# Optimization experiments

Hardware: AMD Instinct MI355X
Metric: run time of the kernel (lower is better)

Reference implementation:

```python
import jax, jax.numpy as jnp
import numpy as np

B, T, NX, H = 2, 2048, 1024, 16
D = NX // H  # head dim = 64
NEG = -1e9


def setup_inputs() -> dict:
    key = jax.random.key(0)
    ks = jax.random.split(key, 4)
    std = 0.02
    x = jax.random.normal(ks[0], (B, T, NX), dtype=jnp.float32)
    # non-trivial adjacency (lower-triangular) so the masking branch is active
    adj = jnp.tril(jnp.ones((T, T), dtype=jnp.float32))
    w_attn = jax.random.normal(ks[1], (NX, 3 * NX), dtype=jnp.float32) * std
    b_attn = jnp.zeros((3 * NX,), dtype=jnp.float32)
    w_proj = jax.random.normal(ks[2], (NX, NX), dtype=jnp.float32) * std
    b_proj = jnp.zeros((NX,), dtype=jnp.float32)
    w_proj1 = jax.random.normal(ks[3], (NX, NX), dtype=jnp.float32) * std
    b_proj1 = jnp.zeros((NX,), dtype=jnp.float32)
    return {"x": x, "adj": adj, "w_attn": w_attn, "b_attn": b_attn,
            "w_proj": w_proj, "b_proj": b_proj,
            "w_proj1": w_proj1, "b_proj1": b_proj1}


def reference(x, adj, w_attn, b_attn, w_proj, b_proj, w_proj1, b_proj1):
    # c_attn: fused qkv projection  [B,T,3*NX]
    qkv = jnp.einsum('btn,nm->btm', x, w_attn) + b_attn
    q, k, v = jnp.split(qkv, 3, axis=-1)  # each [B,T,NX]

    def heads(t):  # [B,T,NX] -> [B,H,T,D]
        return t.reshape(B, T, H, D).transpose(0, 2, 1, 3)

    qh, kh, vh = heads(q), heads(k), heads(v)
    # scale=False in module default: raw dot-product scores
    w = jnp.einsum('bhqd,bhkd->bhqk', qh, kh)  # [B,H,T,T]
    w = w * adj + NEG * (1.0 - adj)            # custom adjacency mask
    w = jax.nn.softmax(w, axis=-1)
    a = jnp.einsum('bhqk,bhkd->bhqd', w, vh)   # [B,H,T,D]
    a = a.transpose(0, 2, 1, 3).reshape(B, T, NX)  # merge heads
    a = jnp.einsum('btn,nm->btm', a, w_proj) + b_proj
    # residue branch: split+merge of query is identity -> c_proj_1(q)
    re = jnp.einsum('btn,nm->btm', q, w_proj1) + b_proj1
    return a + re
```

## Files before the change

### kernel.cpp

```cpp
#include <hip/hip_runtime.h>
#include <stdint.h>

typedef short s16x8 __attribute__((ext_vector_type(8)));
typedef float f32x4 __attribute__((ext_vector_type(4)));
typedef unsigned int u32x4 __attribute__((ext_vector_type(4)));

#define AS1 __attribute__((address_space(1)))
#define AS3 __attribute__((address_space(3)))

static constexpr int Bc = 2, Tc = 2048, NXc = 1024, Hc = 16;
static constexpr float NEGC = -1e9f;
static constexpr float L2E = 1.44269504088896340736f;
static constexpr float LN2 = 0.69314718055994530942f;

static __device__ __forceinline__ unsigned short f2bf(float f) {
  uint32_t u = __builtin_bit_cast(uint32_t, f);
  u += 0x7fffu + ((u >> 16) & 1u);
  return (unsigned short)(u >> 16);
}

static __device__ __forceinline__ float exp2fast(float x) {
  return __builtin_amdgcn_exp2f(x);
}

static __device__ __forceinline__ uint32_t cvt_pk_bf16(float lo, float hi) {
  uint32_t r;
  asm("v_cvt_pk_bf16_f32 %0, %1, %2" : "=v"(r) : "v"(lo), "v"(hi));
  return r;
}

static __device__ __forceinline__ void gload_lds16(const void* g, void* l) {
  __builtin_amdgcn_global_load_lds((const AS1 uint32_t*)g, (AS3 uint32_t*)l, 16, 0, 0);
}

__global__ __launch_bounds__(256) void k_prep(
    const float* __restrict__ x, unsigned short* __restrict__ xb,
    const float* __restrict__ w_attn, unsigned short* __restrict__ wattnT,
    const float* __restrict__ w_proj, const float* __restrict__ w_proj1,
    unsigned short* __restrict__ wcatT,
    const float* __restrict__ adj, unsigned char* __restrict__ tm) {
  __shared__ float tile[32][33];
  __shared__ int s_any, s_all;
  const int bid = blockIdx.x;
  const int t = threadIdx.x;

  if (bid < 4096) {
    int i = bid * 256 + t;
    float4 v = ((const float4*)x)[i];
    uint32_t lo = (uint32_t)f2bf(v.x) | ((uint32_t)f2bf(v.y) << 16);
    uint32_t hi = (uint32_t)f2bf(v.z) | ((uint32_t)f2bf(v.w) << 16);
    ((uint2*)xb)[i] = make_uint2(lo, hi);
    return;
  }
  if (bid < 9216) {
    const float* src; unsigned short* dst;
    int scols, dld, dkoff, n0, k0; float scale;
    if (bid < 7168) {
      int b = bid - 4096; n0 = (b % 96) * 32; k0 = (b / 96) * 32;
      src = w_attn; scols = 3072; dst = wattnT; dld = 1024; dkoff = 0; scale = 1.0f;
    } else if (bid < 8192) {
      int b = bid - 7168; n0 = (b & 31) * 32; k0 = (b >> 5) * 32;
      src = w_proj; scols = 1024; dst = wcatT; dld = 2048; dkoff = 0; scale = 1.0f;
    } else {
      int b = bid - 8192; n0 = (b & 31) * 32; k0 = (b >> 5) * 32;
      src = w_proj1; scols = 1024; dst = wcatT; dld = 2048; dkoff = 1024; scale = LN2;
    }
    int tx = t & 31, ty = t >> 5;
#pragma unroll
    for (int r = 0; r < 4; r++)
      tile[ty + r * 8][tx] = src[(size_t)(k0 + ty + r * 8) * scols + n0 + tx];
    __syncthreads();
#pragma unroll
    for (int r = 0; r < 4; r++) {
      int n = n0 + ty + r * 8;
      dst[(size_t)n * dld + dkoff + k0 + tx] = f2bf(tile[tx][ty + r * 8] * scale);
    }
    return;
  }
  {
    int b = bid - 9216;
    int kt = b & 31, qt = b >> 5;
    bool anyv = false, all1 = true;
#pragma unroll
    for (int i = 0; i < 4; i++) {
      int e = t * 4 + i;
      int row = e >> 4, c4 = e & 15;
      float4 v = *(const float4*)&adj[(size_t)(qt * 64 + row) * Tc + kt * 64 + c4 * 4];
      anyv |= (v.x != 0.f) | (v.y != 0.f) | (v.z != 0.f) | (v.w != 0.f);
      all1 &= (v.x == 1.f) & (v.y == 1.f) & (v.z == 1.f) & (v.w == 1.f);
    }
    if (t == 0) { s_any = 0; s_all = 1; }
    __syncthreads();
    if (anyv) s_any = 1;
    if (!all1) s_all = 0;
    __syncthreads();
    if (t == 0) tm[qt * 32 + kt] = (unsigned char)(s_any ? (s_all ? 2 : 1) : 0);
  }
}

__global__ __launch_bounds__(256) void k_gemm0(
    const unsigned short* __restrict__ A, int lda,
    const unsigned short* __restrict__ BT, int K,
    const float* __restrict__ bias0, unsigned short* __restrict__ Cb) {
  __shared__ __align__(16) unsigned short As[2][128 * 32];
  __shared__ __align__(16) unsigned short Bs[2][128 * 32];
  const int nbx = gridDim.x, nby = gridDim.y;
  const int nwg = nbx * nby;
  int id = blockIdx.y * nbx + blockIdx.x;
  id = (id & 7) * (nwg >> 3) + (id >> 3);
  const int bx = id % nbx;
  const int by = id / nbx;
  const int m0 = by * 128;
  const int n0 = bx * 128;

  const int lane = threadIdx.x & 63;
  const int w = threadIdx.x >> 6;
  const int wr = (w >> 1) * 64;
  const int wc = (w & 1) * 64;
  const int g = lane >> 4, lr = lane & 15;
  const int srow = lane >> 2;
  const int scol = lane & 3;
  f32x4 acc[4][4] = {};

  auto stage = [&](int k0, int buf) {
#pragma unroll
    for (int i = 0; i < 2; i++) {
      int c = w * 2 + i;
      int row = c * 16 + srow;
      int cs = scol ^ (row & 3);
      gload_lds16(A + (size_t)(m0 + row) * lda + k0 + cs * 8, (void*)(&As[buf][0] + c * 512));
      gload_lds16(BT + (size_t)(n0 + row) * K + k0 + cs * 8, (void*)(&Bs[buf][0] + c * 512));
    }
  };

  stage(0, 0);
  __syncthreads();

  for (int k0 = 0; k0 < K; k0 += 32) {
    const int cur = (k0 >> 5) & 1;
    if (k0 + 32 < K) stage(k0 + 32, cur ^ 1);
    s16x8 af[4], bfr[4];
#pragma unroll
    for (int m = 0; m < 4; m++) {
      int row = wr + m * 16 + lr;
      af[m] = *(const s16x8*)((const char*)&As[cur][0] + row * 64 + ((g ^ (row & 3)) * 16));
    }
#pragma unroll
    for (int n = 0; n < 4; n++) {
      int row = wc + n * 16 + lr;
      bfr[n] = *(const s16x8*)((const char*)&Bs[cur][0] + row * 64 + ((g ^ (row & 3)) * 16));
    }
#pragma unroll
    for (int m = 0; m < 4; m++)
#pragma unroll
      for (int n = 0; n < 4; n++)
        acc[m][n] = __builtin_amdgcn_mfma_f32_16x16x32_bf16(af[m], bfr[n], acc[m][n], 0, 0, 0);
    __syncthreads();
  }

#pragma unroll
  for (int m = 0; m < 4; m++) {
    int row = m0 + wr + m * 16 + g * 4;
#pragma unroll
    for (int n = 0; n < 4; n++) {
      int col = n0 + wc + n * 16 + lr;
      float bs = bias0[col];
      float sc = (col < NXc) ? L2E : 1.0f;
#pragma unroll
      for (int jj = 0; jj < 4; jj++)
        Cb[(size_t)(row + jj) * 3072 + col] = f2bf((acc[m][n][jj] + bs) * sc);
    }
  }
}

__global__ __launch_bounds__(256) void k_gemm1(
    const unsigned short* __restrict__ A, int lda,
    const unsigned short* __restrict__ A2, int lda2,
    const unsigned short* __restrict__ BT,
    const float* __restrict__ bias0, const float* __restrict__ bias1,
    float* __restrict__ Cf) {
  constexpr int K = 2048, ksplit = 1024;
  __shared__ __align__(16) unsigned short As[2][64 * 32];
  __shared__ __align__(16) unsigned short Bs[2][128 * 32];
  const int nbx = gridDim.x, nby = gridDim.y;
  const int nwg = nbx * nby;
  int id = blockIdx.y * nbx + blockIdx.x;
  id = (id & 7) * (nwg >> 3) + (id >> 3);
  const int bx = id % nbx;
  const int by = id / nbx;
  const int m0 = by * 64;
  const int n0 = bx * 128;

  const int tid = threadIdx.x;
  const int lane = tid & 63;
  const int w = tid >> 6;
  const int wr = (w >> 1) * 32;
  const int wc = (w & 1) * 64;
  const int g = lane >> 4, lr = lane & 15;
  const int srow = lane >> 2;
  const int scol = lane & 3;
  const int arow = tid >> 2;
  f32x4 acc[2][4] = {};

  auto stage = [&](int k0, int buf) {
    {
      int acs = (tid & 3) ^ (arow & 3);
      const unsigned short* ap = (k0 < ksplit)
          ? A + (size_t)(m0 + arow) * lda + k0
          : A2 + (size_t)(m0 + arow) * lda2 + (k0 - ksplit);
      gload_lds16(ap + acs * 8, (void*)(&As[buf][0] + w * 512));
    }
#pragma unroll
    for (int i = 0; i < 2; i++) {
      int c = w * 2 + i;
      int row = c * 16 + srow;
      int cs = scol ^ (row & 3);
      gload_lds16(BT + (size_t)(n0 + row) * K + k0 + cs * 8, (void*)(&Bs[buf][0] + c * 512));
    }
  };

  stage(0, 0);
  __syncthreads();

  for (int k0 = 0; k0 < K; k0 += 32) {
    const int cur = (k0 >> 5) & 1;
    if (k0 + 32 < K) stage(k0 + 32, cur ^ 1);
    s16x8 af[2], bfr[4];
#pragma unroll
    for (int m = 0; m < 2; m++) {
      int row = wr + m * 16 + lr;
      af[m] = *(const s16x8*)((const char*)&As[cur][0] + row * 64 + ((g ^ (row & 3)) * 16));
    }
#pragma unroll
    for (int n = 0; n < 4; n++) {
      int row = wc + n * 16 + lr;
      bfr[n] = *(const s16x8*)((const char*)&Bs[cur][0] + row * 64 + ((g ^ (row & 3)) * 16));
    }
#pragma unroll
    for (int m = 0; m < 2; m++)
#pragma unroll
      for (int n = 0; n < 4; n++)
        acc[m][n] = __builtin_amdgcn_mfma_f32_16x16x32_bf16(af[m], bfr[n], acc[m][n], 0, 0, 0);
    __syncthreads();
  }

#pragma unroll
  for (int m = 0; m < 2; m++) {
    int row = m0 + wr + m * 16 + g * 4;
#pragma unroll
    for (int n = 0; n < 4; n++) {
      int col = n0 + wc + n * 16 + lr;
      float bs = bias0[col] + bias1[col];
#pragma unroll
      for (int jj = 0; jj < 4; jj++)
        Cf[(size_t)(row + jj) * NXc + col] = acc[m][n][jj] + bs;
    }
  }
}

__global__ __launch_bounds__(256) void k_attn(
    const unsigned short* __restrict__ qkv,
    const float* __restrict__ adj,
    const unsigned char* __restrict__ tm,
    unsigned short* __restrict__ acat) {
  __shared__ __align__(16) unsigned short Kb[2][64 * 64];
  __shared__ __align__(16) unsigned short Vt[2][64 * 72];
  __shared__ int s_kts[34];
  __shared__ unsigned char s_tmv[32];
  __shared__ int s_nkt;

  const int bid = blockIdx.x;
  const int qt = 31 - (bid >> 5);
  const int bh = bid & 31;
  const int h = bh & 15;
  const int b = bh >> 4;
  const int q0 = qt * 64;
  const int tid = threadIdx.x;
  const int lane = tid & 63;
  const int w = tid >> 6;
  const int g = lane >> 4, lr = lane & 15;
  const int sc = tid & 7;
  const int sr = tid >> 3;
  const int kvp = 2 * sr;
  const int prp = (kvp & 32) | (((kvp >> 4) & 1) << 2) | ((kvp & 12) << 1) | (kvp & 3);

  if (w == 0) {
    int kt = lane & 31;
    unsigned char v = tm[qt * 32 + kt];
    bool act = (lane < 32) && (v != 0);
    unsigned long long mk = __ballot(act);
    int n = __popcll(mk);
    if (act) {
      int idx = __popcll(mk & ((1ull << lane) - 1));
      s_kts[idx] = kt;
      s_tmv[idx] = v;
      if (idx == n - 1) { s_kts[n] = kt; s_kts[n + 1] = kt; }
    }
    if (lane == 0) s_nkt = n;
  }

  s16x8 qf0, qf1;
  {
    size_t base = (size_t)(b * Tc + q0 + w * 16 + lr) * 3072 + h * 64 + g * 8;
    qf0 = *(const s16x8*)(qkv + base);
    qf1 = *(const s16x8*)(qkv + base + 32);
  }
  f32x4 o[4] = {};
  float lrow = 0.f;

  __syncthreads();
  const int nkt = s_nkt;
  if (nkt == 0) return;

  const unsigned short* kbase = qkv + (size_t)(b * Tc) * 3072 + 1024 + h * 64;
  const unsigned short* vbase = kbase + 1024;

  const size_t koff0 = (size_t)sr * 3072 + (sc ^ (sr & 7)) * 8;
  const size_t koff1 = (size_t)(sr + 32) * 3072 + (sc ^ (sr & 7)) * 8;
  const int kd0 = w * 1024 + lane * 16;
  const int kd1 = kd0 + 4096;
  const size_t voff0 = (size_t)kvp * 3072 + sc * 8;
  const size_t voff1 = (size_t)(kvp + 1) * 3072 + sc * 8;
  const int pcol = ((prp + sc * 8) & 63) * 2;

  s16x8 kA0, kA1, vA0, vA1;
  auto load_tile = [&](int kt) {
    const unsigned short* kb = kbase + (size_t)kt * 64 * 3072;
    const unsigned short* vb = vbase + (size_t)kt * 64 * 3072;
    kA0 = *(const s16x8*)(kb + koff0);
    kA1 = *(const s16x8*)(kb + koff1);
    vA0 = *(const s16x8*)(vb + voff0);
    vA1 = *(const s16x8*)(vb + voff1);
  };
  auto write_tile = [&](int buf) {
    *(s16x8*)((char*)&Kb[buf][0] + kd0) = kA0;
    *(s16x8*)((char*)&Kb[buf][0] + kd1) = kA1;
    char* vt = (char*)&Vt[buf][0];
#pragma unroll
    for (int j = 0; j < 8; j++) {
      int d = sc * 8 + j;
      uint32_t pk = (uint32_t)(unsigned short)vA0[j] |
                    ((uint32_t)(unsigned short)vA1[j] << 16);
      *(uint32_t*)(vt + d * 144 + pcol) = pk;
    }
  };

  load_tile(s_kts[0]);
  write_tile(0);
  load_tile(s_kts[1]);
  __syncthreads();

  for (int i = 0; i < nkt; i++) {
    const int cur = i & 1;
    const int kt = s_kts[i];
    const int tmv = s_tmv[i];
    const int kv0 = kt * 64;

    write_tile(cur ^ 1);
    load_tile(s_kts[i + 2]);

    f32x4 s[4];
    __builtin_amdgcn_s_setprio(1);
#pragma unroll
    for (int n = 0; n < 4; n++) {
      int kvr = n * 16 + lr;
      const char* kr = (const char*)&Kb[cur][0] + kvr * 128;
      s16x8 a0 = *(const s16x8*)(kr + ((g ^ (kvr & 7)) * 16));
      s16x8 a1 = *(const s16x8*)(kr + (((4 + g) ^ (kvr & 7)) * 16));
      f32x4 z = {};
      z = __builtin_amdgcn_mfma_f32_16x16x32_bf16(a0, qf0, z, 0, 0, 0);
      s[n] = __builtin_amdgcn_mfma_f32_16x16x32_bf16(a1, qf1, z, 0, 0, 0);
    }
    __builtin_amdgcn_s_setprio(0);

    if (tmv != 2) {
      const float* arow = adj + (size_t)(q0 + w * 16 + lr) * Tc + kv0;
#pragma unroll
      for (int n = 0; n < 4; n++) {
        float4 a = *(const float4*)(arow + n * 16 + 4 * g);
        s[n][0] = a.x * s[n][0] + NEGC * (1.0f - a.x);
        s[n][1] = a.y * s[n][1] + NEGC * (1.0f - a.y);
        s[n][2] = a.z * s[n][2] + NEGC * (1.0f - a.z);
        s[n][3] = a.w * s[n][3] + NEGC * (1.0f - a.w);
      }
    }

    float ps0 = 0.f, ps1 = 0.f;
#pragma unroll
    for (int n = 0; n < 4; n++) {
      float p0 = exp2fast(s[n][0]), p1 = exp2fast(s[n][1]);
      float p2 = exp2fast(s[n][2]), p3 = exp2fast(s[n][3]);
      s[n][0] = p0; s[n][1] = p1; s[n][2] = p2; s[n][3] = p3;
      ps0 += (p0 + p1); ps1 += (p2 + p3);
    }
    lrow += ps0 + ps1;

    u32x4 pw0, pw1;
    pw0.x = cvt_pk_bf16(s[0][0], s[0][1]);
    pw0.y = cvt_pk_bf16(s[0][2], s[0][3]);
    pw0.z = cvt_pk_bf16(s[1][0], s[1][1]);
    pw0.w = cvt_pk_bf16(s[1][2], s[1][3]);
    pw1.x = cvt_pk_bf16(s[2][0], s[2][1]);
    pw1.y = cvt_pk_bf16(s[2][2], s[2][3]);
    pw1.z = cvt_pk_bf16(s[3][0], s[3][1]);
    pw1.w = cvt_pk_bf16(s[3][2], s[3][3]);
    s16x8 pa0 = __builtin_bit_cast(s16x8, pw0);
    s16x8 pa1 = __builtin_bit_cast(s16x8, pw1);

    __builtin_amdgcn_s_setprio(1);
#pragma unroll
    for (int nd = 0; nd < 4; nd++) {
      int d = nd * 16 + lr;
      const char* vrow = (const char*)&Vt[cur][0] + d * 144;
      int swz = (d >> 3) * 8;
      s16x8 vb0 = *(const s16x8*)(vrow + (((8 * g + swz) & 63) * 2));
      s16x8 vb1 = *(const s16x8*)(vrow + (((32 + 8 * g + swz) & 63) * 2));
      o[nd] = __builtin_amdgcn_mfma_f32_16x16x32_bf16(pa0, vb0, o[nd], 0, 0, 0);
      o[nd] = __builtin_amdgcn_mfma_f32_16x16x32_bf16(pa1, vb1, o[nd], 0, 0, 0);
    }
    __builtin_amdgcn_s_setprio(0);

    __syncthreads();
  }

  lrow += __shfl_xor(lrow, 16);
  lrow += __shfl_xor(lrow, 32);
  float inv = lrow > 0.f ? 1.0f / lrow : 0.f;
#pragma unroll
  for (int jj = 0; jj < 4; jj++) {
    float iv = __shfl(inv, 4 * g + jj);
    size_t m = (size_t)(b * Tc + q0 + w * 16 + g * 4 + jj);
#pragma unroll
    for (int nd = 0; nd < 4; nd++)
      acat[m * 1024 + h * 64 + nd * 16 + lr] = f2bf(o[nd][jj] * iv);
  }
}

extern "C" void kernel_launch(void* const* d_in, const int* in_sizes, int n_in,
                              void* d_out, int out_size, void* d_ws, size_t ws_size,
                              hipStream_t stream) {
  const float* x       = (const float*)d_in[0];
  const float* adj     = (const float*)d_in[1];
  const float* w_attn  = (const float*)d_in[2];
  const float* b_attn  = (const float*)d_in[3];
  const float* w_proj  = (const float*)d_in[4];
  const float* b_proj  = (const float*)d_in[5];
  const float* w_proj1 = (const float*)d_in[6];
  const float* b_proj1 = (const float*)d_in[7];
  float* out = (float*)d_out;

  char* ws = (char*)d_ws;
  size_t off = 0;
  unsigned short* xb     = (unsigned short*)(ws + off); off += (size_t)4096 * 1024 * 2;
  unsigned short* wattnT = (unsigned short*)(ws + off); off += (size_t)3072 * 1024 * 2;
  unsigned short* wcatT  = (unsigned short*)(ws + off); off += (size_t)1024 * 2048 * 2;
  unsigned short* qkv    = (unsigned short*)(ws + off); off += (size_t)4096 * 3072 * 2;
  unsigned short* acat   = (unsigned short*)(ws + off); off += (size_t)4096 * 1024 * 2;
  unsigned char*  tmask  = (unsigned char*)(ws + off);  off += 1024;
  (void)ws_size; (void)in_sizes; (void)n_in; (void)out_size;

  k_prep<<<10240, 256, 0, stream>>>(x, xb, w_attn, wattnT, w_proj, w_proj1, wcatT,
                                    adj, tmask);
  k_gemm0<<<dim3(24, 32), 256, 0, stream>>>(xb, 1024, wattnT, 1024, b_attn, qkv);
  k_attn<<<1024, 256, 0, stream>>>(qkv, adj, tmask, acat);
  k_gemm1<<<dim3(8, 64), 256, 0, stream>>>(acat, 1024, qkv, 3072,
                                           wcatT, b_proj, b_proj1, out);
}
```

Baseline: 120.2 us.

## Replace direct global-to-LDS loads with register-staged prefetch pipeline in GEMM

The GEMM mainloop no longer uses direct global-to-LDS 16-byte loads. It loads the next-next K tile into registers, writes the previously loaded tile into the alternate LDS buffer, and precomputes address offsets outside the loop. This aims to hide global latency two stages ahead and cut per-iteration address arithmetic, at the cost of extra VGPRs and explicit LDS stores. The final iterations redundantly reload the last tile.

```diff
diff --git a/kernel.cpp b/kernel.cpp
--- a/kernel.cpp
+++ b/kernel.cpp
@@ -200,31 +200,41 @@
   const int srow = lane >> 2;
   const int scol = lane & 3;
   const int arow = tid >> 2;
+  const int acs = (tid & 3) ^ (arow & 3);
+  const int brow0 = (w * 2) * 16 + srow, brow1 = (w * 2 + 1) * 16 + srow;
+  const int bcs0 = scol ^ (brow0 & 3), bcs1 = scol ^ (brow1 & 3);
+  const size_t boff0 = (size_t)(n0 + brow0) * K + bcs0 * 8;
+  const size_t boff1 = (size_t)(n0 + brow1) * K + bcs1 * 8;
+  const int ad = w * 1024 + lane * 16;
+  const int bd0 = (w * 2) * 1024 + lane * 16;
+  const int bd1 = (w * 2 + 1) * 1024 + lane * 16;
+
+  s16x8 aR, bR0, bR1;
+  auto load_t = [&](int k0) {
+    const unsigned short* ap = (k0 < ksplit)
+        ? A + (size_t)(m0 + arow) * lda + k0
+        : A2 + (size_t)(m0 + arow) * lda2 + (k0 - ksplit);
+    aR  = *(const s16x8*)(ap + acs * 8);
+    bR0 = *(const s16x8*)(BT + boff0 + k0);
+    bR1 = *(const s16x8*)(BT + boff1 + k0);
+  };
+  auto write_t = [&](int buf) {
+    *(s16x8*)((char*)&As[buf][0] + ad)  = aR;
+    *(s16x8*)((char*)&Bs[buf][0] + bd0) = bR0;
+    *(s16x8*)((char*)&Bs[buf][0] + bd1) = bR1;
+  };
+
   f32x4 acc[2][4] = {};
 
-  auto stage = [&](int k0, int buf) {
-    {
-      int acs = (tid & 3) ^ (arow & 3);
-      const unsigned short* ap = (k0 < ksplit)
-          ? A + (size_t)(m0 + arow) * lda + k0
-          : A2 + (size_t)(m0 + arow) * lda2 + (k0 - ksplit);
-      gload_lds16(ap + acs * 8, (void*)(&As[buf][0] + w * 512));
-    }
-#pragma unroll
-    for (int i = 0; i < 2; i++) {
-      int c = w * 2 + i;
-      int row = c * 16 + srow;
-      int cs = scol ^ (row & 3);
-      gload_lds16(BT + (size_t)(n0 + row) * K + k0 + cs * 8, (void*)(&Bs[buf][0] + c * 512));
-    }
-  };
-
-  stage(0, 0);
+  load_t(0);
+  write_t(0);
+  load_t(32);
   __syncthreads();
 
   for (int k0 = 0; k0 < K; k0 += 32) {
     const int cur = (k0 >> 5) & 1;
-    if (k0 + 32 < K) stage(k0 + 32, cur ^ 1);
+    write_t(cur ^ 1);
+    load_t(min(k0 + 64, K - 32));
     s16x8 af[2], bfr[4];
 #pragma unroll
     for (int m = 0; m < 2; m++) {
```

Result: no change. 118.8 us (median of 2 runs) (-1.2%).
